# Optimization experiments

Hardware: AMD Instinct MI355X
Metric: run time of the kernel (lower is better)

Reference implementation:

```python
import jax, jax.numpy as jnp
import numpy as np
from math import sqrt

NQ, NV = 4096, 4096
QIN = KIN = VIN = 1024
NHEADS, DK = 8, 512
HEAD_DIM = DK // NHEADS  # 64


def setup_inputs() -> dict:
    key = jax.random.key(0)
    k1, k2, k3, k4, k5, k6 = jax.random.split(key, 6)
    qin = jax.random.normal(k1, (NQ, QIN), dtype=jnp.float32)
    kin = jax.random.normal(k2, (NV, KIN), dtype=jnp.float32)
    vin = jax.random.normal(k3, (NV, VIN), dtype=jnp.float32)
    # Parameters initialized as randn / (head_dim * in_dim), matching the torch module.
    Wqs = jax.random.normal(k4, (NHEADS, HEAD_DIM, QIN), dtype=jnp.float32) / (HEAD_DIM * QIN)
    Wks = jax.random.normal(k5, (NHEADS, HEAD_DIM, KIN), dtype=jnp.float32) / (HEAD_DIM * KIN)
    Wvs = jax.random.normal(k6, (NHEADS, HEAD_DIM, VIN), dtype=jnp.float32) / (HEAD_DIM * VIN)
    return {"qin": qin, "kin": kin, "vin": vin, "Wqs": Wqs, "Wks": Wks, "Wvs": Wvs}


def reference(qin, kin, vin, Wqs, Wks, Wvs):
    # Per-head projections: [h, seq, head_dim]
    Qs = jnp.einsum('qi,hoi->hqo', qin, Wqs)
    Ks = jnp.einsum('ki,hoi->hko', kin, Wks)
    Vs = jnp.einsum('vi,hoi->hvo', vin, Wvs)
    scale = 1.0 / sqrt(HEAD_DIM)  # original divides by sqrt(Q.shape[-1]) = head_dim
    scores = jnp.einsum('hqo,hko->hqk', Qs, Ks) * scale  # [h, nq, nv]
    attn = jax.nn.softmax(scores, axis=-1)
    out = jnp.einsum('hqk,hko->hqo', attn, Vs)           # [h, nq, head_dim]
    # concat over heads along last dim -> [nq, nheads*head_dim]
    return jnp.transpose(out, (1, 0, 2)).reshape(out.shape[1], NHEADS * HEAD_DIM)
```

## Files before the change

### kernel.cpp

```cpp
#include <hip/hip_runtime.h>
#include <hip/hip_bf16.h>

#define NQ 4096
#define NKV 4096
#define DIN 1024
#define NH 8
#define HD 64
#define DMODEL 512
#define NSPLIT 4
#define KVQ (NKV / NSPLIT)
#define QBLK 128

typedef __attribute__((ext_vector_type(4))) float f32x4;
typedef __attribute__((ext_vector_type(8))) short short8;

#define GPTR(p) ((const __attribute__((address_space(1))) void*)(p))
#define SPTR(p) ((__attribute__((address_space(3))) void*)(p))
#define SWZ(r) ((((r) ^ ((r) >> 3)) & 7) << 3)

#define SM_SCALE 0.1803368801111204f

__device__ __forceinline__ ushort f2b(float f) {
  uint u = __float_as_uint(f);
  u = (u + 0x7fffu + ((u >> 16) & 1u)) >> 16;
  return (ushort)u;
}

__device__ __forceinline__ uint cvt_pk_bf16(float lo, float hi) {
  uint r;
  asm("v_cvt_pk_bf16_f32 %0, %1, %2" : "=v"(r) : "v"(lo), "v"(hi));
  return r;
}

__device__ __forceinline__ float fast_exp2(float x) {
  float r;
  asm("v_exp_f32 %0, %1" : "=v"(r) : "v"(x));
  return r;
}

__device__ __forceinline__ float red_max4(float x) {
  float a, b;
  asm("v_mov_b32 %0, %2\n\t"
      "v_mov_b32 %1, %2\n\t"
      "v_permlane32_swap_b32 %0, %1"
      : "=&v"(a), "=&v"(b)
      : "v"(x));
  const float m1 = fmaxf(a, b);
  float c, d;
  asm("v_mov_b32 %0, %2\n\t"
      "v_mov_b32 %1, %2\n\t"
      "v_permlane16_swap_b32 %0, %1"
      : "=&v"(c), "=&v"(d)
      : "v"(m1));
  return fmaxf(c, d);
}

__device__ __forceinline__ float red_sum4(float x) {
  float a, b;
  asm("v_mov_b32 %0, %2\n\t"
      "v_mov_b32 %1, %2\n\t"
      "v_permlane32_swap_b32 %0, %1"
      : "=&v"(a), "=&v"(b)
      : "v"(x));
  const float s = a + b;
  float c, d;
  asm("v_mov_b32 %0, %2\n\t"
      "v_mov_b32 %1, %2\n\t"
      "v_permlane16_swap_b32 %0, %1"
      : "=&v"(c), "=&v"(d)
      : "v"(s));
  return c + d;
}

__global__ void cast3_kernel(const float* __restrict__ s0, const float* __restrict__ s1,
                             const float* __restrict__ s2, ushort* __restrict__ d0,
                             ushort* __restrict__ d1, ushort* __restrict__ d2, int shift) {
  const int n4 = 1 << shift;
  const int total = 3 * n4;
  for (int u = blockIdx.x * blockDim.x + threadIdx.x; u < total;
       u += gridDim.x * blockDim.x) {
    const int a = u >> shift;
    const int off = u & (n4 - 1);
    const float4* src = (const float4*)(a == 0 ? s0 : a == 1 ? s1 : s2);
    ushort* dst = a == 0 ? d0 : a == 1 ? d1 : d2;
    float4 v = src[off];
    ushort4 o = make_ushort4(f2b(v.x), f2b(v.y), f2b(v.z), f2b(v.w));
    ((ushort4*)dst)[off] = o;
  }
}

__global__ __launch_bounds__(256) void proj_gemm(
    const ushort* __restrict__ A0, const ushort* __restrict__ B0, ushort* __restrict__ C0,
    const ushort* __restrict__ A1, const ushort* __restrict__ B1, ushort* __restrict__ C1,
    const ushort* __restrict__ A2, const ushort* __restrict__ B2, ushort* __restrict__ C2) {
  const int z = blockIdx.z;
  const ushort* A = z == 0 ? A0 : z == 1 ? A1 : A2;
  const ushort* B = z == 0 ? B0 : z == 1 ? B1 : B2;
  ushort* C = z == 0 ? C0 : z == 1 ? C1 : C2;

  __shared__ ushort As[64 * 32];
  __shared__ ushort Bs[128 * 32];
  const int tid = threadIdx.x;
  const int w = tid >> 6, lane = tid & 63;
  const int wr = w >> 1, wc = w & 1;
  const int bm = blockIdx.x, bn = blockIdx.y;
  const int l15 = lane & 15, l4 = lane >> 4;

  f32x4 acc[2][4];
#pragma unroll
  for (int m = 0; m < 2; ++m)
#pragma unroll
    for (int n = 0; n < 4; ++n) acc[m][n] = (f32x4){0.f, 0.f, 0.f, 0.f};

  const size_t abase = (size_t)(bm * 64) * DIN;
  const size_t bbase = (size_t)(bn * 128) * DIN;
  const int srow = lane >> 2;
  const int schunk = (lane & 3) * 8;
  const int fcol = l4 * 8;

  for (int k0 = 0; k0 < DIN; k0 += 32) {
    __builtin_amdgcn_global_load_lds(
        GPTR(A + abase + (size_t)(w * 16 + srow) * DIN + k0 + schunk),
        SPTR(As + w * 512), 16, 0, 0);
#pragma unroll
    for (int j = 0; j < 2; ++j) {
      const int slot = w * 2 + j;
      __builtin_amdgcn_global_load_lds(
          GPTR(B + bbase + (size_t)(slot * 16 + srow) * DIN + k0 + schunk),
          SPTR(Bs + slot * 512), 16, 0, 0);
    }
    __syncthreads();
    short8 af[2], bfr[4];
#pragma unroll
    for (int m = 0; m < 2; ++m)
      af[m] = *(const short8*)(As + (wr * 32 + m * 16 + l15) * 32 + fcol);
#pragma unroll
    for (int n = 0; n < 4; ++n)
      bfr[n] = *(const short8*)(Bs + (wc * 64 + n * 16 + l15) * 32 + fcol);
#pragma unroll
    for (int m = 0; m < 2; ++m)
#pragma unroll
      for (int n = 0; n < 4; ++n)
        acc[m][n] = __builtin_amdgcn_mfma_f32_16x16x32_bf16(af[m], bfr[n], acc[m][n], 0, 0, 0);
    __syncthreads();
  }

  const int orow = bm * 64 + wr * 32 + l4 * 4;
  const int ocol = bn * 128 + wc * 64 + l15;
#pragma unroll
  for (int m = 0; m < 2; ++m)
#pragma unroll
    for (int n = 0; n < 4; ++n)
#pragma unroll
      for (int r = 0; r < 4; ++r)
        C[(size_t)(orow + m * 16 + r) * DMODEL + ocol + n * 16] = f2b(acc[m][n][r]);
}

__global__ __launch_bounds__(256, 3) void attn_kernel(
    const ushort* __restrict__ Qp, const ushort* __restrict__ Kp,
    const ushort* __restrict__ Vp, float* __restrict__ Opart,
    float* __restrict__ Mpart, float* __restrict__ Lpart) {
  __shared__ ushort Ks[2][64 * 64];
  __shared__ ushort Vt[2][64 * 64];
  __shared__ ushort Ps[QBLK * 64];
  const int h = blockIdx.y;
  const int q0 = blockIdx.x * QBLK;
  const int split = blockIdx.z;
  const int kvbase = split * KVQ;
  const int tid = threadIdx.x;
  const int w = tid >> 6, lane = tid & 63;
  const int l15 = lane & 15, l4 = lane >> 4;

  const int lrow = lane >> 3, lch = lane & 7;
  int srow[2], sch[2];
#pragma unroll
  for (int j = 0; j < 2; ++j) {
    const int row = (w * 2 + j) * 8 + lrow;
    srow[j] = row;
    sch[j] = (lch ^ ((row ^ (row >> 3)) & 7)) * 8;
  }
  const int vkv = w * 16 + (lane & 7) * 2;
  const int vd0 = ((lane >> 3) & 7) * 8;

#pragma unroll
  for (int j = 0; j < 4; ++j) {
    const int row = (w * 4 + j) * 8 + lrow;
    const int ch = (lch ^ ((row ^ (row >> 3)) & 7)) * 8;
    __builtin_amdgcn_global_load_lds(
        GPTR(Qp + (size_t)(q0 + row) * DMODEL + h * HD + ch),
        SPTR(Ps + (w * 4 + j) * 512), 16, 0, 0);
  }
#pragma unroll
  for (int j = 0; j < 2; ++j)
    __builtin_amdgcn_global_load_lds(
        GPTR(Kp + (size_t)(kvbase + srow[j]) * DMODEL + h * HD + sch[j]),
        SPTR(Ks[0] + (w * 2 + j) * 512), 16, 0, 0);
  short8 vr0 = *(const short8*)(Vp + (size_t)(kvbase + vkv) * DMODEL + h * HD + vd0);
  short8 vr1 = *(const short8*)(Vp + (size_t)(kvbase + vkv + 1) * DMODEL + h * HD + vd0);
  asm volatile("s_waitcnt vmcnt(0)" ::: "memory");
  short8 qa[2][2];
#pragma unroll
  for (int fq = 0; fq < 2; ++fq) {
    const int q = w * 32 + fq * 16 + l15;
    const int sw = SWZ(q);
    qa[fq][0] = *(const short8*)(Ps + q * 64 + ((8 * l4) ^ sw));
    qa[fq][1] = *(const short8*)(Ps + q * 64 + ((32 + 8 * l4) ^ sw));
  }
#pragma unroll
  for (int j = 0; j < 8; ++j) {
    const int d = vd0 + j;
    const uint val = (uint)(ushort)vr0[j] | ((uint)(ushort)vr1[j] << 16);
    *(uint*)(Vt[0] + d * 64 + (vkv ^ SWZ(d))) = val;
  }
  __syncthreads();

  float m_run[2] = {-1e30f, -1e30f}, l_run[2] = {0.f, 0.f};
  f32x4 of[2][4];
#pragma unroll
  for (int fq = 0; fq < 2; ++fq)
#pragma unroll
    for (int fd = 0; fd < 4; ++fd) of[fq][fd] = (f32x4){0.f, 0.f, 0.f, 0.f};

  int cur = 0;
  for (int it = 0; it < KVQ / 64; ++it) {
    short8 pv0, pv1;
    const bool pf = (it + 1) < KVQ / 64;
    if (pf) {
      const int kvn = kvbase + (it + 1) * 64;
#pragma unroll
      for (int j = 0; j < 2; ++j)
        __builtin_amdgcn_global_load_lds(
            GPTR(Kp + (size_t)(kvn + srow[j]) * DMODEL + h * HD + sch[j]),
            SPTR(Ks[cur ^ 1] + (w * 2 + j) * 512), 16, 0, 0);
      pv0 = *(const short8*)(Vp + (size_t)(kvn + vkv) * DMODEL + h * HD + vd0);
      pv1 = *(const short8*)(Vp + (size_t)(kvn + vkv + 1) * DMODEL + h * HD + vd0);
    }

    f32x4 sf[2][4];
#pragma unroll
    for (int fq = 0; fq < 2; ++fq)
#pragma unroll
      for (int fn = 0; fn < 4; ++fn) sf[fq][fn] = (f32x4){0.f, 0.f, 0.f, 0.f};
#pragma unroll
    for (int fn = 0; fn < 4; ++fn) {
      const int kvr = fn * 16 + l15;
      const int sw = SWZ(kvr);
      short8 kb0 = *(const short8*)(Ks[cur] + kvr * 64 + ((8 * l4) ^ sw));
      short8 kb1 = *(const short8*)(Ks[cur] + kvr * 64 + ((32 + 8 * l4) ^ sw));
      sf[0][fn] = __builtin_amdgcn_mfma_f32_16x16x32_bf16(kb0, qa[0][0], sf[0][fn], 0, 0, 0);
      sf[0][fn] = __builtin_amdgcn_mfma_f32_16x16x32_bf16(kb1, qa[0][1], sf[0][fn], 0, 0, 0);
      sf[1][fn] = __builtin_amdgcn_mfma_f32_16x16x32_bf16(kb0, qa[1][0], sf[1][fn], 0, 0, 0);
      sf[1][fn] = __builtin_amdgcn_mfma_f32_16x16x32_bf16(kb1, qa[1][1], sf[1][fn], 0, 0, 0);
    }

#pragma unroll
    for (int fq = 0; fq < 2; ++fq) {
      float t0 = fmaxf(fmaxf(sf[fq][0][0], sf[fq][0][1]), fmaxf(sf[fq][0][2], sf[fq][0][3]));
      float t1 = fmaxf(fmaxf(sf[fq][1][0], sf[fq][1][1]), fmaxf(sf[fq][1][2], sf[fq][1][3]));
      float t2 = fmaxf(fmaxf(sf[fq][2][0], sf[fq][2][1]), fmaxf(sf[fq][2][2], sf[fq][2][3]));
      float t3 = fmaxf(fmaxf(sf[fq][3][0], sf[fq][3][1]), fmaxf(sf[fq][3][2], sf[fq][3][3]));
      float rmax2 = red_max4(fmaxf(fmaxf(t0, t1), fmaxf(t2, t3)) * SM_SCALE);
      if (__any(rmax2 > m_run[fq] + 8.0f)) {
        const float mnew = fmaxf(m_run[fq], rmax2);
        const float alpha = fast_exp2(m_run[fq] - mnew);
        m_run[fq] = mnew;
        l_run[fq] *= alpha;
        float ar[4];
#pragma unroll
        for (int r = 0; r < 4; ++r) ar[r] = __shfl(alpha, l4 * 4 + r);
#pragma unroll
        for (int fd = 0; fd < 4; ++fd)
#pragma unroll
          for (int r = 0; r < 4; ++r) of[fq][fd][r] *= ar[r];
      }
      float rsum = 0.f;
#pragma unroll
      for (int fn = 0; fn < 4; ++fn)
#pragma unroll
        for (int r = 0; r < 4; ++r) {
          const float v = fast_exp2(__builtin_fmaf(sf[fq][fn][r], SM_SCALE, -m_run[fq]));
          sf[fq][fn][r] = v;
          rsum += v;
        }
      l_run[fq] += red_sum4(rsum);
    }

#pragma unroll
    for (int fq = 0; fq < 2; ++fq) {
      const int q = w * 32 + fq * 16 + l15;
      const int sw = SWZ(q);
#pragma unroll
      for (int fn = 0; fn < 4; ++fn) {
        uint2 u;
        u.x = cvt_pk_bf16(sf[fq][fn][0], sf[fq][fn][1]);
        u.y = cvt_pk_bf16(sf[fq][fn][2], sf[fq][fn][3]);
        *(uint2*)(Ps + q * 64 + ((fn * 16 + l4 * 4) ^ sw)) = u;
      }
    }
    asm volatile("s_waitcnt lgkmcnt(0)" ::: "memory");
    __builtin_amdgcn_sched_barrier(0);

    {
      short8 pa[2][2];
#pragma unroll
      for (int fq = 0; fq < 2; ++fq) {
        const int q = w * 32 + fq * 16 + l15;
        const int swp = SWZ(q);
        pa[fq][0] = *(const short8*)(Ps + q * 64 + ((8 * l4) ^ swp));
        pa[fq][1] = *(const short8*)(Ps + q * 64 + ((32 + 8 * l4) ^ swp));
      }
#pragma unroll
      for (int fd = 0; fd < 4; ++fd) {
        const int dr = fd * 16 + l15;
        const int sw = SWZ(dr);
        short8 vb0 = *(const short8*)(Vt[cur] + dr * 64 + ((8 * l4) ^ sw));
        short8 vb1 = *(const short8*)(Vt[cur] + dr * 64 + ((32 + 8 * l4) ^ sw));
        of[0][fd] = __builtin_amdgcn_mfma_f32_16x16x32_bf16(pa[0][0], vb0, of[0][fd], 0, 0, 0);
        of[0][fd] = __builtin_amdgcn_mfma_f32_16x16x32_bf16(pa[0][1], vb1, of[0][fd], 0, 0, 0);
        of[1][fd] = __builtin_amdgcn_mfma_f32_16x16x32_bf16(pa[1][0], vb0, of[1][fd], 0, 0, 0);
        of[1][fd] = __builtin_amdgcn_mfma_f32_16x16x32_bf16(pa[1][1], vb1, of[1][fd], 0, 0, 0);
      }
    }

    if (pf) {
#pragma unroll
      for (int j = 0; j < 8; ++j) {
        const int d = vd0 + j;
        const uint val = (uint)(ushort)pv0[j] | ((uint)(ushort)pv1[j] << 16);
        *(uint*)(Vt[cur ^ 1] + d * 64 + (vkv ^ SWZ(d))) = val;
      }
    }
    __syncthreads();
    cur ^= 1;
  }

#pragma unroll
  for (int fq = 0; fq < 2; ++fq) {
#pragma unroll
    for (int r = 0; r < 4; ++r) {
      const int qrow = q0 + w * 32 + fq * 16 + l4 * 4 + r;
#pragma unroll
      for (int fd = 0; fd < 4; ++fd)
        Opart[(size_t)split * (NQ * DMODEL) + (size_t)qrow * DMODEL + h * HD + fd * 16 + l15] =
            of[fq][fd][r];
    }
    if (l4 == 0) {
      const int qrow = q0 + w * 32 + fq * 16 + l15;
      Mpart[(split * NH + h) * NQ + qrow] = m_run[fq];
      Lpart[(split * NH + h) * NQ + qrow] = l_run[fq];
    }
  }
}

__global__ __launch_bounds__(256) void merge_kernel(
    const float* __restrict__ Opart, const float* __restrict__ Mpart,
    const float* __restrict__ Lpart, float* __restrict__ out) {
  const int i4 = blockIdx.x * 256 + threadIdx.x;
  const int i = i4 * 4;
  const int q = i >> 9;
  const int col = i & 511;
  const int h = col >> 6;
  float m[NSPLIT];
  float mm = -1e30f;
#pragma unroll
  for (int s = 0; s < NSPLIT; ++s) {
    m[s] = Mpart[(s * NH + h) * NQ + q];
    mm = fmaxf(mm, m[s]);
  }
  float l = 0.f, ws[NSPLIT];
#pragma unroll
  for (int s = 0; s < NSPLIT; ++s) {
    ws[s] = fast_exp2(m[s] - mm);
    l += ws[s] * Lpart[(s * NH + h) * NQ + q];
  }
  const float inv = 1.0f / l;
  float4 o = {0.f, 0.f, 0.f, 0.f};
#pragma unroll
  for (int s = 0; s < NSPLIT; ++s) {
    const float4 os = ((const float4*)(Opart + (size_t)s * NQ * DMODEL))[i4];
    o.x += ws[s] * os.x;
    o.y += ws[s] * os.y;
    o.z += ws[s] * os.z;
    o.w += ws[s] * os.w;
  }
  o.x *= inv; o.y *= inv; o.z *= inv; o.w *= inv;
  ((float4*)out)[i4] = o;
}

extern "C" void kernel_launch(void* const* d_in, const int* in_sizes, int n_in,
                              void* d_out, int out_size, void* d_ws, size_t ws_size,
                              hipStream_t stream) {
  const float* qin = (const float*)d_in[0];
  const float* kin = (const float*)d_in[1];
  const float* vin = (const float*)d_in[2];
  const float* Wq = (const float*)d_in[3];
  const float* Wk = (const float*)d_in[4];
  const float* Wv = (const float*)d_in[5];
  float* out = (float*)d_out;

  char* ws = (char*)d_ws;
  const size_t MB = 1 << 20;
  ushort* Qp = (ushort*)(ws + 0 * MB);
  ushort* Kp = (ushort*)(ws + 4 * MB);
  ushort* Vp = (ushort*)(ws + 8 * MB);
  ushort* qb = (ushort*)(ws + 12 * MB);
  ushort* kb = (ushort*)(ws + 20 * MB);
  ushort* vb = (ushort*)(ws + 28 * MB);
  ushort* wqb = (ushort*)(ws + 36 * MB);
  ushort* wkb = (ushort*)(ws + 37 * MB);
  ushort* wvb = (ushort*)(ws + 38 * MB);
  float* Opart = (float*)(ws + 12 * MB);
  float* Mpart = (float*)(ws + 44 * MB);
  float* Lpart = (float*)(ws + 44 * MB + 512 * 1024);

  cast3_kernel<<<2048, 256, 0, stream>>>(qin, kin, vin, qb, kb, vb, 20);
  cast3_kernel<<<1536, 256, 0, stream>>>(Wq, Wk, Wv, wqb, wkb, wvb, 17);
  proj_gemm<<<dim3(64, 4, 3), 256, 0, stream>>>(qb, wqb, Qp, kb, wkb, Kp, vb, wvb, Vp);
  attn_kernel<<<dim3(NQ / QBLK, NH, NSPLIT), 256, 0, stream>>>(Qp, Kp, Vp, Opart, Mpart, Lpart);
  merge_kernel<<<(NQ * DMODEL / 4) / 256, 256, 0, stream>>>(Opart, Mpart, Lpart, out);
}
```

Before: 198.1 us.

## Keep P in registers via permlane swaps, double-buffer projection GEMM, compute row sums with MFMA

The attention kernel no longer writes P to LDS and reads it back. It repacks the bf16 probabilities in registers with permlane32/16 swaps and swaps the MFMA operand order so the output is transposed. The row sum l is now computed by an extra MFMA against a ones vector instead of cross-lane reductions. Dropping the Ps buffer frees LDS, so occupancy goes up to 4 blocks, with Q staged through the K buffer. The projection GEMM is separately rewritten to use a double-buffered 64-wide K tile with a swizzled LDS layout, adding more MFMA work and register pressure in exchange.

```diff
diff --git a/kernel.cpp b/kernel.cpp
--- a/kernel.cpp
+++ b/kernel.cpp
@@ -10,6 +10,7 @@
 #define NSPLIT 4
 #define KVQ (NKV / NSPLIT)
 #define QBLK 128
+#define NT (KVQ / 64)
 
 typedef __attribute__((ext_vector_type(4))) float f32x4;
 typedef __attribute__((ext_vector_type(8))) short short8;
@@ -55,22 +56,14 @@
   return fmaxf(c, d);
 }
 
-__device__ __forceinline__ float red_sum4(float x) {
-  float a, b;
-  asm("v_mov_b32 %0, %2\n\t"
-      "v_mov_b32 %1, %2\n\t"
-      "v_permlane32_swap_b32 %0, %1"
-      : "=&v"(a), "=&v"(b)
-      : "v"(x));
-  const float s = a + b;
-  float c, d;
-  asm("v_mov_b32 %0, %2\n\t"
-      "v_mov_b32 %1, %2\n\t"
-      "v_permlane16_swap_b32 %0, %1"
-      : "=&v"(c), "=&v"(d)
-      : "v"(s));
-  return c + d;
-}
+__device__ __forceinline__ void plane32_swap(uint& a, uint& b) {
+  asm("v_permlane32_swap_b32 %0, %1" : "+v"(a), "+v"(b));
+}
+__device__ __forceinline__ void plane16_swap(uint& a, uint& b) {
+  asm("v_permlane16_swap_b32 %0, %1" : "+v"(a), "+v"(b));
+}
+
+union U4S8 { uint4 u; short8 s; };
 
 __global__ void cast3_kernel(const float* __restrict__ s0, const float* __restrict__ s1,
                              const float* __restrict__ s2, ushort* __restrict__ d0,
@@ -98,13 +91,14 @@
   const ushort* B = z == 0 ? B0 : z == 1 ? B1 : B2;
   ushort* C = z == 0 ? C0 : z == 1 ? C1 : C2;
 
-  __shared__ ushort As[64 * 32];
-  __shared__ ushort Bs[128 * 32];
+  __shared__ ushort As[2][64 * 64];
+  __shared__ ushort Bs[2][128 * 64];
   const int tid = threadIdx.x;
   const int w = tid >> 6, lane = tid & 63;
   const int wr = w >> 1, wc = w & 1;
   const int bm = blockIdx.x, bn = blockIdx.y;
   const int l15 = lane & 15, l4 = lane >> 4;
+  const int lrow = lane >> 3, lch = lane & 7;
 
   f32x4 acc[2][4];
 #pragma unroll
@@ -114,35 +108,72 @@
 
   const size_t abase = (size_t)(bm * 64) * DIN;
   const size_t bbase = (size_t)(bn * 128) * DIN;
-  const int srow = lane >> 2;
-  const int schunk = (lane & 3) * 8;
-  const int fcol = l4 * 8;
-
-  for (int k0 = 0; k0 < DIN; k0 += 32) {
-    __builtin_amdgcn_global_load_lds(
-        GPTR(A + abase + (size_t)(w * 16 + srow) * DIN + k0 + schunk),
-        SPTR(As + w * 512), 16, 0, 0);
-#pragma unroll
-    for (int j = 0; j < 2; ++j) {
-      const int slot = w * 2 + j;
-      __builtin_amdgcn_global_load_lds(
-          GPTR(B + bbase + (size_t)(slot * 16 + srow) * DIN + k0 + schunk),
-          SPTR(Bs + slot * 512), 16, 0, 0);
-    }
+
+  int arow[2], ach[2];
+#pragma unroll
+  for (int j = 0; j < 2; ++j) {
+    const int row = (w * 2 + j) * 8 + lrow;
+    arow[j] = row;
+    ach[j] = (lch ^ ((row ^ (row >> 3)) & 7)) * 8;
+  }
+  int brow[4], bch[4];
+#pragma unroll
+  for (int j = 0; j < 4; ++j) {
+    const int row = (w * 4 + j) * 8 + lrow;
+    brow[j] = row;
+    bch[j] = (lch ^ ((row ^ (row >> 3)) & 7)) * 8;
+  }
+
+#pragma unroll
+  for (int j = 0; j < 2; ++j)
+    __builtin_amdgcn_global_load_lds(GPTR(A + abase + (size_t)arow[j] * DIN + ach[j]),
+                                     SPTR(As[0] + (w * 2 + j) * 512), 16, 0, 0);
+#pragma unroll
+  for (int j = 0; j < 4; ++j)
+    __builtin_amdgcn_global_load_lds(GPTR(B + bbase + (size_t)brow[j] * DIN + bch[j]),
+                                     SPTR(Bs[0] + (w * 4 + j) * 512), 16, 0, 0);
+  __syncthreads();
+
+  int cur = 0;
+  for (int it = 0; it < DIN / 64; ++it) {
+    if (it + 1 < DIN / 64) {
+      const int k0 = (it + 1) * 64;
+#pragma unroll
+      for (int j = 0; j < 2; ++j)
+        __builtin_amdgcn_global_load_lds(
+            GPTR(A + abase + (size_t)arow[j] * DIN + k0 + ach[j]),
+            SPTR(As[cur ^ 1] + (w * 2 + j) * 512), 16, 0, 0);
+#pragma unroll
+      for (int j = 0; j < 4; ++j)
+        __builtin_amdgcn_global_load_lds(
+            GPTR(B + bbase + (size_t)brow[j] * DIN + k0 + bch[j]),
+            SPTR(Bs[cur ^ 1] + (w * 4 + j) * 512), 16, 0, 0);
+    }
+    short8 af[2][2], bfr[4][2];
+#pragma unroll
+    for (int m = 0; m < 2; ++m) {
+      const int row = wr * 32 + m * 16 + l15;
+      const int sw = SWZ(row);
+      af[m][0] = *(const short8*)(As[cur] + row * 64 + ((8 * l4) ^ sw));
+      af[m][1] = *(const short8*)(As[cur] + row * 64 + ((32 + 8 * l4) ^ sw));
+    }
+#pragma unroll
+    for (int n = 0; n < 4; ++n) {
+      const int row = wc * 64 + n * 16 + l15;
+      const int sw = SWZ(row);
+      bfr[n][0] = *(const short8*)(Bs[cur] + row * 64 + ((8 * l4) ^ sw));
+      bfr[n][1] = *(const short8*)(Bs[cur] + row * 64 + ((32 + 8 * l4) ^ sw));
+    }
+#pragma unroll
+    for (int ks = 0; ks < 2; ++ks)
+#pragma unroll
+      for (int m = 0; m < 2; ++m)
+#pragma unroll
+        for (int n = 0; n < 4; ++n)
+          acc[m][n] =
+              __builtin_amdgcn_mfma_f32_16x16x32_bf16(af[m][ks], bfr[n][ks], acc[m][n], 0, 0, 0);
     __syncthreads();
-    short8 af[2], bfr[4];
-#pragma unroll
-    for (int m = 0; m < 2; ++m)
-      af[m] = *(const short8*)(As + (wr * 32 + m * 16 + l15) * 32 + fcol);
-#pragma unroll
-    for (int n = 0; n < 4; ++n)
-      bfr[n] = *(const short8*)(Bs + (wc * 64 + n * 16 + l15) * 32 + fcol);
-#pragma unroll
-    for (int m = 0; m < 2; ++m)
-#pragma unroll
-      for (int n = 0; n < 4; ++n)
-        acc[m][n] = __builtin_amdgcn_mfma_f32_16x16x32_bf16(af[m], bfr[n], acc[m][n], 0, 0, 0);
-    __syncthreads();
+    cur ^= 1;
   }
 
   const int orow = bm * 64 + wr * 32 + l4 * 4;
@@ -156,13 +187,12 @@
         C[(size_t)(orow + m * 16 + r) * DMODEL + ocol + n * 16] = f2b(acc[m][n][r]);
 }
 
-__global__ __launch_bounds__(256, 3) void attn_kernel(
+__global__ __launch_bounds__(256, 4) void attn_kernel(
     const ushort* __restrict__ Qp, const ushort* __restrict__ Kp,
     const ushort* __restrict__ Vp, float* __restrict__ Opart,
     float* __restrict__ Mpart, float* __restrict__ Lpart) {
   __shared__ ushort Ks[2][64 * 64];
   __shared__ ushort Vt[2][64 * 64];
-  __shared__ ushort Ps[QBLK * 64];
   const int h = blockIdx.y;
   const int q0 = blockIdx.x * QBLK;
   const int split = blockIdx.z;
@@ -170,8 +200,8 @@
   const int tid = threadIdx.x;
   const int w = tid >> 6, lane = tid & 63;
   const int l15 = lane & 15, l4 = lane >> 4;
-
   const int lrow = lane >> 3, lch = lane & 7;
+
   int srow[2], sch[2];
 #pragma unroll
   for (int j = 0; j < 2; ++j) {
@@ -182,30 +212,32 @@
   const int vkv = w * 16 + (lane & 7) * 2;
   const int vd0 = ((lane >> 3) & 7) * 8;
 
+  short8 vr0 = *(const short8*)(Vp + (size_t)(kvbase + vkv) * DMODEL + h * HD + vd0);
+  short8 vr1 = *(const short8*)(Vp + (size_t)(kvbase + vkv + 1) * DMODEL + h * HD + vd0);
+  ushort* Qstage = &Ks[0][0];
 #pragma unroll
   for (int j = 0; j < 4; ++j) {
     const int row = (w * 4 + j) * 8 + lrow;
     const int ch = (lch ^ ((row ^ (row >> 3)) & 7)) * 8;
     __builtin_amdgcn_global_load_lds(
         GPTR(Qp + (size_t)(q0 + row) * DMODEL + h * HD + ch),
-        SPTR(Ps + (w * 4 + j) * 512), 16, 0, 0);
-  }
+        SPTR(Qstage + (w * 4 + j) * 512), 16, 0, 0);
+  }
+  asm volatile("s_waitcnt vmcnt(0)" ::: "memory");
+  short8 qa[2][2];
+#pragma unroll
+  for (int fq = 0; fq < 2; ++fq) {
+    const int q = w * 32 + fq * 16 + l15;
+    const int sw = SWZ(q);
+    qa[fq][0] = *(const short8*)(Qstage + q * 64 + ((8 * l4) ^ sw));
+    qa[fq][1] = *(const short8*)(Qstage + q * 64 + ((32 + 8 * l4) ^ sw));
+  }
+  __syncthreads();
 #pragma unroll
   for (int j = 0; j < 2; ++j)
     __builtin_amdgcn_global_load_lds(
         GPTR(Kp + (size_t)(kvbase + srow[j]) * DMODEL + h * HD + sch[j]),
         SPTR(Ks[0] + (w * 2 + j) * 512), 16, 0, 0);
-  short8 vr0 = *(const short8*)(Vp + (size_t)(kvbase + vkv) * DMODEL + h * HD + vd0);
-  short8 vr1 = *(const short8*)(Vp + (size_t)(kvbase + vkv + 1) * DMODEL + h * HD + vd0);
-  asm volatile("s_waitcnt vmcnt(0)" ::: "memory");
-  short8 qa[2][2];
-#pragma unroll
-  for (int fq = 0; fq < 2; ++fq) {
-    const int q = w * 32 + fq * 16 + l15;
-    const int sw = SWZ(q);
-    qa[fq][0] = *(const short8*)(Ps + q * 64 + ((8 * l4) ^ sw));
-    qa[fq][1] = *(const short8*)(Ps + q * 64 + ((32 + 8 * l4) ^ sw));
-  }
 #pragma unroll
   for (int j = 0; j < 8; ++j) {
     const int d = vd0 + j;
@@ -214,17 +246,27 @@
   }
   __syncthreads();
 
-  float m_run[2] = {-1e30f, -1e30f}, l_run[2] = {0.f, 0.f};
+  short8 ones;
+  {
+    const short ov = (l15 == 0) ? (short)0x3F80 : (short)0;
+#pragma unroll
+    for (int j = 0; j < 8; ++j) ones[j] = ov;
+  }
+
+  float m_run[2] = {-1e30f, -1e30f};
   f32x4 of[2][4];
-#pragma unroll
-  for (int fq = 0; fq < 2; ++fq)
+  f32x4 of_l[2];
+#pragma unroll
+  for (int fq = 0; fq < 2; ++fq) {
+    of_l[fq] = (f32x4){0.f, 0.f, 0.f, 0.f};
 #pragma unroll
     for (int fd = 0; fd < 4; ++fd) of[fq][fd] = (f32x4){0.f, 0.f, 0.f, 0.f};
+  }
 
   int cur = 0;
-  for (int it = 0; it < KVQ / 64; ++it) {
+  for (int it = 0; it < NT; ++it) {
     short8 pv0, pv1;
-    const bool pf = (it + 1) < KVQ / 64;
+    const bool pf = (it + 1) < NT;
     if (pf) {
       const int kvn = kvbase + (it + 1) * 64;
 #pragma unroll
@@ -253,74 +295,71 @@
       sf[1][fn] = __builtin_amdgcn_mfma_f32_16x16x32_bf16(kb1, qa[1][1], sf[1][fn], 0, 0, 0);
     }
 
+    short8 pb[2][2];
 #pragma unroll
     for (int fq = 0; fq < 2; ++fq) {
       float t0 = fmaxf(fmaxf(sf[fq][0][0], sf[fq][0][1]), fmaxf(sf[fq][0][2], sf[fq][0][3]));
       float t1 = fmaxf(fmaxf(sf[fq][1][0], sf[fq][1][1]), fmaxf(sf[fq][1][2], sf[fq][1][3]));
       float t2 = fmaxf(fmaxf(sf[fq][2][0], sf[fq][2][1]), fmaxf(sf[fq][2][2], sf[fq][2][3]));
       float t3 = fmaxf(fmaxf(sf[fq][3][0], sf[fq][3][1]), fmaxf(sf[fq][3][2], sf[fq][3][3]));
-      float rmax2 = red_max4(fmaxf(fmaxf(t0, t1), fmaxf(t2, t3)) * SM_SCALE);
+      const float rmax2 = red_max4(fmaxf(fmaxf(t0, t1), fmaxf(t2, t3)) * SM_SCALE);
       if (__any(rmax2 > m_run[fq] + 8.0f)) {
         const float mnew = fmaxf(m_run[fq], rmax2);
         const float alpha = fast_exp2(m_run[fq] - mnew);
         m_run[fq] = mnew;
-        l_run[fq] *= alpha;
-        float ar[4];
-#pragma unroll
-        for (int r = 0; r < 4; ++r) ar[r] = __shfl(alpha, l4 * 4 + r);
 #pragma unroll
         for (int fd = 0; fd < 4; ++fd)
 #pragma unroll
-          for (int r = 0; r < 4; ++r) of[fq][fd][r] *= ar[r];
+          for (int r = 0; r < 4; ++r) of[fq][fd][r] *= alpha;
+#pragma unroll
+        for (int r = 0; r < 4; ++r) of_l[fq][r] *= alpha;
       }
-      float rsum = 0.f;
 #pragma unroll
       for (int fn = 0; fn < 4; ++fn)
 #pragma unroll
-        for (int r = 0; r < 4; ++r) {
-          const float v = fast_exp2(__builtin_fmaf(sf[fq][fn][r], SM_SCALE, -m_run[fq]));
-          sf[fq][fn][r] = v;
-          rsum += v;
-        }
-      l_run[fq] += red_sum4(rsum);
-    }
-
-#pragma unroll
-    for (int fq = 0; fq < 2; ++fq) {
-      const int q = w * 32 + fq * 16 + l15;
-      const int sw = SWZ(q);
-#pragma unroll
-      for (int fn = 0; fn < 4; ++fn) {
-        uint2 u;
-        u.x = cvt_pk_bf16(sf[fq][fn][0], sf[fq][fn][1]);
-        u.y = cvt_pk_bf16(sf[fq][fn][2], sf[fq][fn][3]);
-        *(uint2*)(Ps + q * 64 + ((fn * 16 + l4 * 4) ^ sw)) = u;
+        for (int r = 0; r < 4; ++r)
+          sf[fq][fn][r] = fast_exp2(__builtin_fmaf(sf[fq][fn][r], SM_SCALE, -m_run[fq]));
+      uint u00 = cvt_pk_bf16(sf[fq][0][0], sf[fq][0][1]);
+      uint u01 = cvt_pk_bf16(sf[fq][0][2], sf[fq][0][3]);
+      uint u10 = cvt_pk_bf16(sf[fq][1][0], sf[fq][1][1]);
+      uint u11 = cvt_pk_bf16(sf[fq][1][2], sf[fq][1][3]);
+      uint u20 = cvt_pk_bf16(sf[fq][2][0], sf[fq][2][1]);
+      uint u21 = cvt_pk_bf16(sf[fq][2][2], sf[fq][2][3]);
+      uint u30 = cvt_pk_bf16(sf[fq][3][0], sf[fq][3][1]);
+      uint u31 = cvt_pk_bf16(sf[fq][3][2], sf[fq][3][3]);
+      {
+        uint a = u00, b = u10;
+        plane32_swap(a, b); plane16_swap(a, b);
+        uint a1 = u01, b1 = u11;
+        plane32_swap(a1, b1); plane16_swap(a1, b1);
+        U4S8 t; t.u = make_uint4(a, a1, b, b1);
+        pb[fq][0] = t.s;
       }
-    }
-    asm volatile("s_waitcnt lgkmcnt(0)" ::: "memory");
-    __builtin_amdgcn_sched_barrier(0);
-
-    {
-      short8 pa[2][2];
-#pragma unroll
-      for (int fq = 0; fq < 2; ++fq) {
-        const int q = w * 32 + fq * 16 + l15;
-        const int swp = SWZ(q);
-        pa[fq][0] = *(const short8*)(Ps + q * 64 + ((8 * l4) ^ swp));
-        pa[fq][1] = *(const short8*)(Ps + q * 64 + ((32 + 8 * l4) ^ swp));
+      {
+        uint a = u20, b = u30;
+        plane32_swap(a, b); plane16_swap(a, b);
+        uint a1 = u21, b1 = u31;
+        plane32_swap(a1, b1); plane16_swap(a1, b1);
+        U4S8 t; t.u = make_uint4(a, a1, b, b1);
+        pb[fq][1] = t.s;
       }
-#pragma unroll
-      for (int fd = 0; fd < 4; ++fd) {
-        const int dr = fd * 16 + l15;
-        const int sw = SWZ(dr);
-        short8 vb0 = *(const short8*)(Vt[cur] + dr * 64 + ((8 * l4) ^ sw));
-        short8 vb1 = *(const short8*)(Vt[cur] + dr * 64 + ((32 + 8 * l4) ^ sw));
-        of[0][fd] = __builtin_amdgcn_mfma_f32_16x16x32_bf16(pa[0][0], vb0, of[0][fd], 0, 0, 0);
-        of[0][fd] = __builtin_amdgcn_mfma_f32_16x16x32_bf16(pa[0][1], vb1, of[0][fd], 0, 0, 0);
-        of[1][fd] = __builtin_amdgcn_mfma_f32_16x16x32_bf16(pa[1][0], vb0, of[1][fd], 0, 0, 0);
-        of[1][fd] = __builtin_amdgcn_mfma_f32_16x16x32_bf16(pa[1][1], vb1, of[1][fd], 0, 0, 0);
-      }
-    }
+    }
+
+#pragma unroll
+    for (int fd = 0; fd < 4; ++fd) {
+      const int dr = fd * 16 + l15;
+      const int sw = SWZ(dr);
+      short8 vb0 = *(const short8*)(Vt[cur] + dr * 64 + ((8 * l4) ^ sw));
+      short8 vb1 = *(const short8*)(Vt[cur] + dr * 64 + ((32 + 8 * l4) ^ sw));
+      of[0][fd] = __builtin_amdgcn_mfma_f32_16x16x32_bf16(vb0, pb[0][0], of[0][fd], 0, 0, 0);
+      of[0][fd] = __builtin_amdgcn_mfma_f32_16x16x32_bf16(vb1, pb[0][1], of[0][fd], 0, 0, 0);
+      of[1][fd] = __builtin_amdgcn_mfma_f32_16x16x32_bf16(vb0, pb[1][0], of[1][fd], 0, 0, 0);
+      of[1][fd] = __builtin_amdgcn_mfma_f32_16x16x32_bf16(vb1, pb[1][1], of[1][fd], 0, 0, 0);
+    }
+    of_l[0] = __builtin_amdgcn_mfma_f32_16x16x32_bf16(ones, pb[0][0], of_l[0], 0, 0, 0);
+    of_l[0] = __builtin_amdgcn_mfma_f32_16x16x32_bf16(ones, pb[0][1], of_l[0], 0, 0, 0);
+    of_l[1] = __builtin_amdgcn_mfma_f32_16x16x32_bf16(ones, pb[1][0], of_l[1], 0, 0, 0);
+    of_l[1] = __builtin_amdgcn_mfma_f32_16x16x32_bf16(ones, pb[1][1], of_l[1], 0, 0, 0);
 
     if (pf) {
 #pragma unroll
@@ -336,18 +375,14 @@
 
 #pragma unroll
   for (int fq = 0; fq < 2; ++fq) {
-#pragma unroll
-    for (int r = 0; r < 4; ++r) {
-      const int qrow = q0 + w * 32 + fq * 16 + l4 * 4 + r;
-#pragma unroll
-      for (int fd = 0; fd < 4; ++fd)
-        Opart[(size_t)split * (NQ * DMODEL) + (size_t)qrow * DMODEL + h * HD + fd * 16 + l15] =
-            of[fq][fd][r];
-    }
+    const int q = q0 + w * 32 + fq * 16 + l15;
+    float* orow = Opart + (size_t)split * (NQ * DMODEL) + (size_t)q * DMODEL + h * HD;
+#pragma unroll
+    for (int fd = 0; fd < 4; ++fd)
+      *(float4*)(orow + fd * 16 + l4 * 4) = *(float4*)&of[fq][fd];
     if (l4 == 0) {
-      const int qrow = q0 + w * 32 + fq * 16 + l15;
-      Mpart[(split * NH + h) * NQ + qrow] = m_run[fq];
-      Lpart[(split * NH + h) * NQ + qrow] = l_run[fq];
+      Mpart[(split * NH + h) * NQ + q] = m_run[fq];
+      Lpart[(split * NH + h) * NQ + q] = of_l[fq][0];
     }
   }
 }
```

New measurement: 191.7 us. 3.3% less time.
